# Kernel optimization log

Measured on AMD Instinct MI355X. Metric: run time of the kernel, lower is better.

The kernel has to match this reference:

```python
import jax, jax.numpy as jnp
import numpy as np

N_HEADS = 8
D_EMBED = 512
D_HEAD = D_EMBED // N_HEADS


def setup_inputs() -> dict:
    key = jax.random.key(0)
    ks = jax.random.split(key, 5)
    B, S, D = 8, 2048, D_EMBED
    scale_in = 1.0 / np.sqrt(D)
    x = jax.random.normal(ks[0], (B, S, D), dtype=jnp.float32)
    # torch nn.Linear weights: (out_features, in_features)
    w_in = jax.random.normal(ks[1], (3 * D, D), dtype=jnp.float32) * scale_in
    b_in = jax.random.normal(ks[2], (3 * D,), dtype=jnp.float32) * scale_in
    w_out = jax.random.normal(ks[3], (D, D), dtype=jnp.float32) * scale_in
    b_out = jax.random.normal(ks[4], (D,), dtype=jnp.float32) * scale_in
    return {"x": x, "w_in": w_in, "b_in": b_in, "w_out": w_out, "b_out": b_out}


def reference(x, w_in, b_in, w_out, b_out):
    B, S, D = x.shape
    H, Dh = N_HEADS, D_HEAD
    # fused QKV projection (torch Linear: x @ W^T + b)
    qkv = x @ w_in.T + b_in                     # (B, S, 3D)
    q, k, v = jnp.split(qkv, 3, axis=-1)        # each (B, S, D)
    # split heads -> (B, H, S, Dh)
    def heads(t):
        return t.reshape(B, S, H, Dh).transpose(0, 2, 1, 3)
    q, k, v = heads(q), heads(k), heads(v)
    # scaled dot-product attention (full matrix, as in source)
    scores = jnp.einsum("bhqd,bhkd->bhqk", q, k) / jnp.sqrt(jnp.float32(Dh))
    weights = jax.nn.softmax(scores, axis=-1)   # (B, H, S, S)
    out = jnp.einsum("bhqk,bhkd->bhqd", weights, v)
    out = out.transpose(0, 2, 1, 3).reshape(B, S, D)
    return out @ w_out.T + b_out
```

## Files before the change

### kernel.cpp

```cpp
#include <hip/hip_runtime.h>
#include <stdint.h>

#define SEQ   2048
#define DEMB  512
#define NH    8
#define DH    64
#define BATCH 8
#define M_ROWS (BATCH * SEQ)
#define QKLD  1024
#define PSLD  72
#define QSCALE 0.18033688011112042f

typedef __attribute__((ext_vector_type(8))) __bf16 bf16x8;
typedef __attribute__((ext_vector_type(4))) __bf16 bf16x4;
typedef __attribute__((ext_vector_type(4))) float  f32x4;
typedef __attribute__((ext_vector_type(8))) uint16_t u16x8;

__device__ __forceinline__ void gll16(const __bf16* g, __bf16* l) {
    __builtin_amdgcn_global_load_lds(
        (__attribute__((address_space(1))) void*)(__bf16*)g,
        (__attribute__((address_space(3))) void*)l, 16, 0, 0);
}

__device__ __forceinline__ bf16x8 ld8(const __bf16* p) {
    return *(const bf16x8*)p;
}

__device__ __forceinline__ uint32_t pkbf(float a, float b) {
    uint32_t ua = __builtin_bit_cast(uint32_t, a) + 0x8000u;
    uint32_t ub = __builtin_bit_cast(uint32_t, b) + 0x8000u;
    return __builtin_amdgcn_perm(ub, ua, 0x07060302);
}

__device__ __forceinline__ int sw(int row, int chunk) {
    return row * 64 + ((chunk ^ (row & 7)) << 3);
}

__device__ __forceinline__ void stage_gll_sw(const __bf16* g, int gld,
                                             __bf16* l, int wave, int lane) {
    const int lr = lane >> 3;
    const int scol = ((lane & 7) ^ lr) * 8;
    #pragma unroll
    for (int i = 0; i < 2; i++) {
        const int r0 = i * 32 + wave * 8;
        gll16(g + (size_t)(r0 + lr) * gld + scol, l + r0 * 64);
    }
}

__device__ __forceinline__ void stage_gll(const __bf16* src, __bf16* dst,
                                          int ld, int wave, int lane) {
    const int srow = lane >> 3, scol = (lane & 7) * 8;
    #pragma unroll
    for (int i = 0; i < 4; i++) {
        const int r0 = (i * 4 + wave) * 8;
        gll16(src + (size_t)(r0 + srow) * ld + scol, dst + r0 * 64);
    }
}

#define NXQ (M_ROWS * DEMB / 4)
#define NWQ (3 * DEMB * DEMB / 4)
#define NOQ (DEMB * DEMB / 4)

__global__ __launch_bounds__(256)
void cvt_all(const float* __restrict__ x, const float* __restrict__ w_in,
             __bf16* __restrict__ xb, __bf16* __restrict__ wb) {
    const int i = blockIdx.x * 256 + threadIdx.x;
    const float4* src;
    bf16x4* dst;
    if (i < NXQ) { src = (const float4*)x + i;         dst = (bf16x4*)xb + i; }
    else if (i < NXQ + NWQ) {
        const int j = i - NXQ;
        src = (const float4*)w_in + j;  dst = (bf16x4*)wb + j;
    } else return;
    const float4 v = *src;
    bf16x4 b;
    b[0] = (__bf16)v.x; b[1] = (__bf16)v.y;
    b[2] = (__bf16)v.z; b[3] = (__bf16)v.w;
    *dst = b;
}

__global__ __launch_bounds__(256)
void cvt_wout(const float* __restrict__ w, __bf16* __restrict__ wb) {
    const int i = blockIdx.x * 256 + threadIdx.x;
    if (i < NOQ) {
        const float4 v = ((const float4*)w)[i];
        bf16x4 b;
        b[0] = (__bf16)v.x; b[1] = (__bf16)v.y;
        b[2] = (__bf16)v.z; b[3] = (__bf16)v.w;
        ((bf16x4*)wb)[i] = b;
    }
}

__global__ __launch_bounds__(256)
void gemm_qkv(const __bf16* __restrict__ A, const __bf16* __restrict__ W,
              const float* __restrict__ bias, __bf16* __restrict__ qk,
              __bf16* __restrict__ vt) {
    constexpr int K = DEMB;
    __shared__ __align__(16) __bf16 As[128 * 64];
    __shared__ __align__(16) __bf16 Bs[128 * 64];

    const int tid  = threadIdx.x;
    const int wave = tid >> 6, lane = tid & 63;
    const int quad = lane >> 4, l16 = lane & 15;
    const int m0 = blockIdx.x * 128, n0 = blockIdx.y * 128;
    const int wm = wave & 1, wn = wave >> 1;

    f32x4 acc[4][4] = {};

    for (int k0 = 0; k0 < K; k0 += 64) {
        __syncthreads();
        stage_gll(A + (size_t)m0 * K + k0, As, K, wave, lane);
        stage_gll(W + (size_t)n0 * K + k0, Bs, K, wave, lane);
        __syncthreads();
        #pragma unroll
        for (int ks = 0; ks < 2; ks++) {
            bf16x8 af[4], bf[4];
            #pragma unroll
            for (int t = 0; t < 4; t++) {
                af[t] = ld8(&As[(wm * 64 + t * 16 + l16) * 64 + ks * 32 + quad * 8]);
                bf[t] = ld8(&Bs[(wn * 64 + t * 16 + l16) * 64 + ks * 32 + quad * 8]);
            }
            #pragma unroll
            for (int i = 0; i < 4; i++)
                #pragma unroll
                for (int j = 0; j < 4; j++)
                    acc[i][j] = __builtin_amdgcn_mfma_f32_16x16x32_bf16(
                        af[i], bf[j], acc[i][j], 0, 0, 0);
        }
    }

    if (n0 < QKLD) {
        const float scl = (n0 < DEMB) ? QSCALE : 1.0f;
        #pragma unroll
        for (int j = 0; j < 4; j++) {
            const int n = n0 + wn * 64 + j * 16 + l16;
            const float bv = bias[n];
            #pragma unroll
            for (int i = 0; i < 4; i++) {
                const int mr = m0 + wm * 64 + i * 16 + quad * 4;
                #pragma unroll
                for (int r = 0; r < 4; r++)
                    qk[(size_t)(mr + r) * QKLD + n] = (__bf16)((acc[i][j][r] + bv) * scl);
            }
        }
    } else {
        #pragma unroll
        for (int j = 0; j < 4; j++) {
            const int n = n0 + wn * 64 + j * 16 + l16;
            const float bv = bias[n];
            const int hd = n - QKLD;
            #pragma unroll
            for (int i = 0; i < 4; i++) {
                const int mr = m0 + wm * 64 + i * 16 + quad * 4;
                const int b = mr >> 11, s = mr & (SEQ - 1);
                bf16x4 pk;
                #pragma unroll
                for (int r = 0; r < 4; r++)
                    pk[r] = (__bf16)(acc[i][j][r] + bv);
                *(bf16x4*)(vt + ((size_t)(b * 512 + hd)) * SEQ + s) = pk;
            }
        }
    }
}

__global__ __launch_bounds__(256)
void attn_flash(const __bf16* __restrict__ qk, const __bf16* __restrict__ vt,
                __bf16* __restrict__ outp) {
    const int qt = blockIdx.x, h = blockIdx.y, b = blockIdx.z;
    const int tid  = threadIdx.x;
    const int wave = tid >> 6, lane = tid & 63;
    const int quad = lane >> 4, l16 = lane & 15;

    __shared__ __align__(16) __bf16 Ks[2][64 * 64];
    __shared__ __align__(16) __bf16 Vt[2][64 * 64];
    __shared__ __align__(16) __bf16 Ps[4][2][16 * PSLD];

    const size_t brow = (size_t)b * SEQ;
    const int q0 = qt * 128 + wave * 32;
    const __bf16* kbase = qk + brow * QKLD + DEMB + h * DH;
    const __bf16* vbase = vt + ((size_t)(b * 512 + h * DH)) * SEQ;

    const u16x8 one16 = {0x3F80, 0x3F80, 0x3F80, 0x3F80,
                         0x3F80, 0x3F80, 0x3F80, 0x3F80};
    const bf16x8 ONES = __builtin_bit_cast(bf16x8, one16);

    bf16x8 qf[2][2];
    #pragma unroll
    for (int qb = 0; qb < 2; qb++) {
        const __bf16* qp = qk + (brow + q0 + qb * 16 + l16) * QKLD + h * DH + quad * 8;
        qf[qb][0] = ld8(qp);
        qf[qb][1] = ld8(qp + 32);
    }

    f32x4 o[2][4] = {};
    f32x4 osum[2] = {};

    stage_gll_sw(kbase, QKLD, Ks[0], wave, lane);
    stage_gll_sw(vbase, SEQ,  Vt[0], wave, lane);

    for (int t = 0; t < SEQ / 64; t++) {
        __syncthreads();
        if (t + 1 < SEQ / 64) {
            const int nb = (t + 1) & 1;
            stage_gll_sw(kbase + (size_t)(t + 1) * 64 * QKLD, QKLD, Ks[nb], wave, lane);
            stage_gll_sw(vbase + (t + 1) * 64,                SEQ,  Vt[nb], wave, lane);
        }
        const int buf = t & 1;

        f32x4 st[2][4];
        #pragma unroll
        for (int kt = 0; kt < 4; kt++) {
            bf16x8 kf0 = ld8(&Ks[buf][sw(kt * 16 + l16, quad)]);
            bf16x8 kf1 = ld8(&Ks[buf][sw(kt * 16 + l16, 4 + quad)]);
            #pragma unroll
            for (int qb = 0; qb < 2; qb++) {
                f32x4 c = {};
                c = __builtin_amdgcn_mfma_f32_16x16x32_bf16(kf0, qf[qb][0], c, 0, 0, 0);
                c = __builtin_amdgcn_mfma_f32_16x16x32_bf16(kf1, qf[qb][1], c, 0, 0, 0);
                st[qb][kt] = c;
            }
        }

        #pragma unroll
        for (int qb = 0; qb < 2; qb++) {
            #pragma unroll
            for (int kt = 0; kt < 4; kt++) {
                const float p0 = exp2f(st[qb][kt][0]);
                const float p1 = exp2f(st[qb][kt][1]);
                const float p2 = exp2f(st[qb][kt][2]);
                const float p3 = exp2f(st[qb][kt][3]);
                uint2 w;
                w.x = pkbf(p0, p1);
                w.y = pkbf(p2, p3);
                *(uint2*)(&Ps[wave][qb][l16 * PSLD + kt * 16 + quad * 4]) = w;
            }
        }

        bf16x8 pf[2][2];
        #pragma unroll
        for (int qb = 0; qb < 2; qb++) {
            pf[qb][0] = ld8(&Ps[wave][qb][l16 * PSLD + quad * 8]);
            pf[qb][1] = ld8(&Ps[wave][qb][l16 * PSLD + 32 + quad * 8]);
            osum[qb] = __builtin_amdgcn_mfma_f32_16x16x32_bf16(pf[qb][0], ONES, osum[qb], 0, 0, 0);
            osum[qb] = __builtin_amdgcn_mfma_f32_16x16x32_bf16(pf[qb][1], ONES, osum[qb], 0, 0, 0);
        }
        #pragma unroll
        for (int db = 0; db < 4; db++) {
            bf16x8 vf0 = ld8(&Vt[buf][sw(db * 16 + l16, quad)]);
            bf16x8 vf1 = ld8(&Vt[buf][sw(db * 16 + l16, 4 + quad)]);
            #pragma unroll
            for (int qb = 0; qb < 2; qb++) {
                o[qb][db] = __builtin_amdgcn_mfma_f32_16x16x32_bf16(pf[qb][0], vf0, o[qb][db], 0, 0, 0);
                o[qb][db] = __builtin_amdgcn_mfma_f32_16x16x32_bf16(pf[qb][1], vf1, o[qb][db], 0, 0, 0);
            }
        }
    }

    #pragma unroll
    for (int qb = 0; qb < 2; qb++)
        #pragma unroll
        for (int r = 0; r < 4; r++) {
            const float linv = 1.f / osum[qb][r];
            const int q = q0 + qb * 16 + quad * 4 + r;
            #pragma unroll
            for (int db = 0; db < 4; db++)
                outp[(brow + q) * DEMB + h * DH + db * 16 + l16] =
                    (__bf16)(o[qb][db][r] * linv);
        }
}

__global__ __launch_bounds__(256)
void gemm_out(const __bf16* __restrict__ A, const __bf16* __restrict__ W,
              const float* __restrict__ bias, float* __restrict__ C,
              int N, int K) {
    __shared__ __align__(16) __bf16 As[128 * 64];
    __shared__ __align__(16) __bf16 Bs[128 * 64];

    const int tid  = threadIdx.x;
    const int wave = tid >> 6, lane = tid & 63;
    const int quad = lane >> 4, l16 = lane & 15;
    const int m0 = blockIdx.x * 128, n0 = blockIdx.y * 128;
    const int wm = wave & 1, wn = wave >> 1;

    f32x4 acc[4][4] = {};

    for (int k0 = 0; k0 < K; k0 += 64) {
        __syncthreads();
        stage_gll(A + (size_t)m0 * K + k0, As, K, wave, lane);
        stage_gll(W + (size_t)n0 * K + k0, Bs, K, wave, lane);
        __syncthreads();
        #pragma unroll
        for (int ks = 0; ks < 2; ks++) {
            bf16x8 af[4], bf[4];
            #pragma unroll
            for (int t = 0; t < 4; t++) {
                af[t] = ld8(&As[(wm * 64 + t * 16 + l16) * 64 + ks * 32 + quad * 8]);
                bf[t] = ld8(&Bs[(wn * 64 + t * 16 + l16) * 64 + ks * 32 + quad * 8]);
            }
            #pragma unroll
            for (int i = 0; i < 4; i++)
                #pragma unroll
                for (int j = 0; j < 4; j++)
                    acc[i][j] = __builtin_amdgcn_mfma_f32_16x16x32_bf16(
                        af[i], bf[j], acc[i][j], 0, 0, 0);
        }
    }

    #pragma unroll
    for (int j = 0; j < 4; j++) {
        const int n = n0 + wn * 64 + j * 16 + l16;
        const float bv = bias[n];
        #pragma unroll
        for (int i = 0; i < 4; i++) {
            const int mr = m0 + wm * 64 + i * 16 + quad * 4;
            #pragma unroll
            for (int r = 0; r < 4; r++)
                C[(size_t)(mr + r) * N + n] = acc[i][j][r] + bv;
        }
    }
}

extern "C" void kernel_launch(void* const* d_in, const int* in_sizes, int n_in,
                              void* d_out, int out_size, void* d_ws, size_t ws_size,
                              hipStream_t stream) {
    const float* x     = (const float*)d_in[0];
    const float* w_in  = (const float*)d_in[1];
    const float* b_in  = (const float*)d_in[2];
    const float* w_out = (const float*)d_in[3];
    const float* b_out = (const float*)d_in[4];

    __bf16* qk   = (__bf16*)d_ws;
    __bf16* vtb  = qk + (size_t)M_ROWS * QKLD;
    __bf16* xbuf = vtb + (size_t)BATCH * DEMB * SEQ;
    __bf16* aout = xbuf;
    __bf16* woutb = vtb;
    __bf16* winb = (__bf16*)((char*)d_out + 24u * 1024 * 1024);
    float*  outp = (float*)d_out;

    cvt_all<<<(NXQ + NWQ + 255) / 256, 256, 0, stream>>>(x, w_in, xbuf, winb);
    gemm_qkv<<<dim3(M_ROWS / 128, 12), 256, 0, stream>>>(xbuf, winb, b_in, qk, vtb);
    attn_flash<<<dim3(SEQ / 128, NH, BATCH), 256, 0, stream>>>(qk, vtb, aout);
    cvt_wout<<<NOQ / 256, 256, 0, stream>>>(w_out, woutb);
    gemm_out<<<dim3(M_ROWS / 128, DEMB / 128), 256, 0, stream>>>(
        aout, woutb, b_out, outp, DEMB, DEMB);
}
```

Baseline: 278.2 us.

## Stage V-transpose through LDS, swizzle P buffer, use native exp2/rcp

The QKV GEMM epilogue for V now writes the tile transposed into a swizzled shared-memory buffer and then emits coalesced 16-byte stores to the transposed V array, instead of scattered 8-byte stores. In attention, the per-wave P scratch is shrunk to one XOR-swizzled 16x64 buffer reused across query blocks, replacing the padded layout. exp2f and the division are replaced by the hardware exp2 and rcp intrinsics. Reusing one P buffer per wave adds a write-after-read dependency between query blocks, and the native intrinsics have slightly lower precision.

```diff
diff --git a/kernel.cpp b/kernel.cpp
--- a/kernel.cpp
+++ b/kernel.cpp
@@ -8,7 +8,6 @@
 #define BATCH 8
 #define M_ROWS (BATCH * SEQ)
 #define QKLD  1024
-#define PSLD  72
 #define QSCALE 0.18033688011112042f
 
 typedef __attribute__((ext_vector_type(8))) __bf16 bf16x8;
@@ -96,8 +95,9 @@
               const float* __restrict__ bias, __bf16* __restrict__ qk,
               __bf16* __restrict__ vt) {
     constexpr int K = DEMB;
-    __shared__ __align__(16) __bf16 As[128 * 64];
-    __shared__ __align__(16) __bf16 Bs[128 * 64];
+    __shared__ __align__(16) __bf16 SM[128 * 128];
+    __bf16* As = SM;
+    __bf16* Bs = SM + 128 * 64;
 
     const int tid  = threadIdx.x;
     const int wave = tid >> 6, lane = tid & 63;
@@ -144,21 +144,34 @@
             }
         }
     } else {
+        __syncthreads();
+        const int hd0 = n0 - QKLD;
+        const int bb = m0 >> 11, s0 = m0 & (SEQ - 1);
         #pragma unroll
         for (int j = 0; j < 4; j++) {
             const int n = n0 + wn * 64 + j * 16 + l16;
             const float bv = bias[n];
-            const int hd = n - QKLD;
+            const int hdl = wn * 64 + j * 16 + l16;
             #pragma unroll
             for (int i = 0; i < 4; i++) {
-                const int mr = m0 + wm * 64 + i * 16 + quad * 4;
-                const int b = mr >> 11, s = mr & (SEQ - 1);
+                const int sl = wm * 64 + i * 16 + quad * 4;
                 bf16x4 pk;
                 #pragma unroll
                 for (int r = 0; r < 4; r++)
                     pk[r] = (__bf16)(acc[i][j][r] + bv);
-                *(bf16x4*)(vt + ((size_t)(b * 512 + hd)) * SEQ + s) = pk;
-            }
+                const int chunk = sl >> 3;
+                const int phys = (((chunk & 7) ^ (hdl & 7)) | (chunk & 8));
+                *(bf16x4*)(&SM[hdl * 128 + phys * 8 + (sl & 7)]) = pk;
+            }
+        }
+        __syncthreads();
+        const int g = tid >> 4, li = tid & 15;
+        #pragma unroll
+        for (int it = 0; it < 8; it++) {
+            const int row = it * 16 + g;
+            const int phys = (((li & 7) ^ (row & 7)) | (li & 8));
+            bf16x8 v = ld8(&SM[row * 128 + phys * 8]);
+            *(bf16x8*)(vt + ((size_t)(bb * DEMB + hd0 + row)) * SEQ + s0 + li * 8) = v;
         }
     }
 }
@@ -173,12 +186,12 @@
 
     __shared__ __align__(16) __bf16 Ks[2][64 * 64];
     __shared__ __align__(16) __bf16 Vt[2][64 * 64];
-    __shared__ __align__(16) __bf16 Ps[4][2][16 * PSLD];
+    __shared__ __align__(16) __bf16 Ps[4][16 * 64];
 
     const size_t brow = (size_t)b * SEQ;
     const int q0 = qt * 128 + wave * 32;
     const __bf16* kbase = qk + brow * QKLD + DEMB + h * DH;
-    const __bf16* vbase = vt + ((size_t)(b * 512 + h * DH)) * SEQ;
+    const __bf16* vbase = vt + ((size_t)(b * DEMB + h * DH)) * SEQ;
 
     const u16x8 one16 = {0x3F80, 0x3F80, 0x3F80, 0x3F80,
                          0x3F80, 0x3F80, 0x3F80, 0x3F80};
@@ -221,29 +234,27 @@
             }
         }
 
+        bf16x8 pf[2][2];
         #pragma unroll
         for (int qb = 0; qb < 2; qb++) {
             #pragma unroll
             for (int kt = 0; kt < 4; kt++) {
-                const float p0 = exp2f(st[qb][kt][0]);
-                const float p1 = exp2f(st[qb][kt][1]);
-                const float p2 = exp2f(st[qb][kt][2]);
-                const float p3 = exp2f(st[qb][kt][3]);
+                const float p0 = __builtin_amdgcn_exp2f(st[qb][kt][0]);
+                const float p1 = __builtin_amdgcn_exp2f(st[qb][kt][1]);
+                const float p2 = __builtin_amdgcn_exp2f(st[qb][kt][2]);
+                const float p3 = __builtin_amdgcn_exp2f(st[qb][kt][3]);
                 uint2 w;
                 w.x = pkbf(p0, p1);
                 w.y = pkbf(p2, p3);
-                *(uint2*)(&Ps[wave][qb][l16 * PSLD + kt * 16 + quad * 4]) = w;
-            }
-        }
-
-        bf16x8 pf[2][2];
-        #pragma unroll
-        for (int qb = 0; qb < 2; qb++) {
-            pf[qb][0] = ld8(&Ps[wave][qb][l16 * PSLD + quad * 8]);
-            pf[qb][1] = ld8(&Ps[wave][qb][l16 * PSLD + 32 + quad * 8]);
+                const int chunk = kt * 2 + (quad >> 1);
+                *(uint2*)(&Ps[wave][l16 * 64 + ((chunk ^ (l16 & 7)) << 3) + (quad & 1) * 4]) = w;
+            }
+            pf[qb][0] = ld8(&Ps[wave][sw(l16, quad)]);
+            pf[qb][1] = ld8(&Ps[wave][sw(l16, 4 + quad)]);
             osum[qb] = __builtin_amdgcn_mfma_f32_16x16x32_bf16(pf[qb][0], ONES, osum[qb], 0, 0, 0);
             osum[qb] = __builtin_amdgcn_mfma_f32_16x16x32_bf16(pf[qb][1], ONES, osum[qb], 0, 0, 0);
         }
+
         #pragma unroll
         for (int db = 0; db < 4; db++) {
             bf16x8 vf0 = ld8(&Vt[buf][sw(db * 16 + l16, quad)]);
@@ -260,7 +271,7 @@
     for (int qb = 0; qb < 2; qb++)
         #pragma unroll
         for (int r = 0; r < 4; r++) {
-            const float linv = 1.f / osum[qb][r];
+            const float linv = __builtin_amdgcn_rcpf(osum[qb][r]);
             const int q = q0 + qb * 16 + quad * 4 + r;
             #pragma unroll
             for (int db = 0; db < 4; db++)
```

After: 261.3 us. 1.06x faster.
